# Optimization experiments

Measured on AMD Instinct MI355X. Metric: run time of the kernel, lower is better.

Reference implementation:

```python
import jax, jax.numpy as jnp
import numpy as np
from jax import lax

STATE_SIZE = 80
HIDDEN = 512
NC = 1
H = W = 32
STEPS = 64  # steps_range=(64,64)
THRESH = 0.01


def _maxpool3(x):
    # MaxPool2d(3, stride=1, padding=1) on NCHW
    return lax.reduce_window(x, -jnp.inf, lax.max, (1, 1, 3, 3), (1, 1, 1, 1), 'SAME')


def _conv3x3(x, w, b):
    y = lax.conv_general_dilated(x, w, (1, 1), 'SAME',
                                 dimension_numbers=('NCHW', 'OIHW', 'NCHW'))
    return y + b[None, :, None, None]


def _conv1x1(x, w, b):
    # w: (O, I, 1, 1) -> pointwise einsum
    return jnp.einsum('oi,bihw->bohw', w[:, :, 0, 0], x) + b[None, :, None, None]


def setup_inputs() -> dict:
    key = jax.random.key(0)
    ks = jax.random.split(key, 7)
    z = jax.random.normal(ks[0], (8, 100, 1, 1), dtype=jnp.float32)
    W1 = jax.random.normal(ks[1], (HIDDEN, STATE_SIZE, 3, 3), jnp.float32) / np.sqrt(STATE_SIZE * 9)
    b1 = jax.random.normal(ks[2], (HIDDEN,), jnp.float32) * 0.01
    W2 = jax.random.normal(ks[3], (HIDDEN, HIDDEN, 1, 1), jnp.float32) / np.sqrt(HIDDEN)
    b2 = jax.random.normal(ks[4], (HIDDEN,), jnp.float32) * 0.01
    # original code zero-inits the last conv; use small random weights so grads flow
    W3 = jax.random.normal(ks[5], (STATE_SIZE, HIDDEN, 1, 1), jnp.float32) * (0.01 / np.sqrt(HIDDEN))
    b3 = jax.random.normal(ks[6], (STATE_SIZE,), jnp.float32) * 0.001
    return {'z': z, 'W1': W1, 'b1': b1, 'W2': W2, 'b2': b2, 'W3': W3, 'b3': b3}


def _forward(z, W1, b1, W2, b2, W3, b3):
    N = z.shape[0]
    cH, cW = H // 2, W // 2
    state = jnp.zeros((N, STATE_SIZE, H, W), dtype=z.dtype)
    init_hidden = z[:, :STATE_SIZE - 1, 0, 0]  # (N, 79)
    state = state.at[:, 1:, cH, cW].set(init_hidden)
    state = state.at[:, 0, cH, cW].set(1.0)

    keys = jax.random.split(jax.random.key(42), STEPS)

    def ca_step(state, step_key):
        pre_living = _maxpool3(state[:, 0:1]) > THRESH
        perception = _conv3x3(state, W1, b1)
        h = jax.nn.relu(_conv1x1(perception, W2, b2))
        updates = _conv1x1(h, W3, b3)
        # stochastic update with p=1 (rand < 1 is always True, kept for fidelity)
        mask = jax.random.uniform(step_key, (state.shape[0], 1, H, W)) < 1.0
        state = state + mask.astype(state.dtype) * updates
        post_living = _maxpool3(state[:, 0:1]) > THRESH
        living = (post_living & pre_living).astype(state.dtype)
        return state * living, None

    state, _ = lax.scan(ca_step, state, keys)
    return state[:, :NC]  # (N, 1, H, W)


def reference(z, W1, b1, W2, b2, W3, b3):
    return _forward(z, W1, b1, W2, b2, W3, b3)
```

## Files before the change

kernel.cpp:

```cpp
#include <hip/hip_runtime.h>


#define NPIX 8192
#define T_ALIVE 0.01f

typedef _Float16 f16;
typedef __attribute__((ext_vector_type(8)))  _Float16 h8_t;
typedef __attribute__((ext_vector_type(4)))  _Float16 h4_t;
typedef __attribute__((ext_vector_type(16))) float    fx16;

__global__ __launch_bounds__(256) void tr512(
    const float* __restrict__ W2, float* __restrict__ W2T)
{
    __shared__ float t[32][33];
    const int bx = blockIdx.x & 15, by = blockIdx.x >> 4;
    const int x = threadIdx.x & 31, y8 = threadIdx.x >> 5;
#pragma unroll
    for (int r = 0; r < 32; r += 8)
        t[r + y8][x] = W2[(size_t)(by * 32 + r + y8) * 512 + bx * 32 + x];
    __syncthreads();
#pragma unroll
    for (int r = 0; r < 32; r += 8)
        W2T[(size_t)(bx * 32 + r + y8) * 512 + by * 32 + x] = t[x][r + y8];
}

__global__ __launch_bounds__(256) void wc32(
    const float* __restrict__ W2T, const float* __restrict__ W1,
    float* __restrict__ Wc)
{
    __shared__ float As[16][32];
    __shared__ float Bs[16][32];
    const int tid = threadIdx.x;
    const int ty = tid >> 3, tx = tid & 7;
    const int m0 = blockIdx.y * 32, n0 = blockIdx.x * 32;
    float acc[4] = {0.f, 0.f, 0.f, 0.f};

    for (int k0 = 0; k0 < 512; k0 += 16) {
#pragma unroll
        for (int t = 0; t < 2; ++t) {
            const int idx = tid + t * 256;
            const int r = idx >> 5, c = idx & 31;
            As[r][c] = W2T[(size_t)(k0 + r) * 512 + m0 + c];
            const int n = n0 + c;
            Bs[r][c] = (n < 720) ? W1[(size_t)(k0 + r) * 720 + n] : 0.f;
        }
        __syncthreads();
#pragma unroll
        for (int kk = 0; kk < 16; ++kk) {
            const float a = As[kk][ty];
#pragma unroll
            for (int j = 0; j < 4; ++j)
                acc[j] = fmaf(a, Bs[kk][tx * 4 + j], acc[j]);
        }
        __syncthreads();
    }
    const int m = m0 + ty;
#pragma unroll
    for (int j = 0; j < 4; ++j) {
        const int n = n0 + tx * 4 + j;
        if (n < 720) Wc[(size_t)m * 720 + n] = acc[j];
    }
}

__global__ __launch_bounds__(256) void bc_k(
    const float* __restrict__ W2, const float* __restrict__ b1,
    const float* __restrict__ b2, float* __restrict__ bc)
{
    const int m = blockIdx.x * 256 + threadIdx.x;
    if (m >= 512) return;
    float a = b2[m];
    for (int h = 0; h < 512; ++h) a += W2[m * 512 + h] * b1[h];
    bc[m] = a;
}

__global__ __launch_bounds__(256) void swz_wc2(
    const float* __restrict__ Wc, f16* __restrict__ Wcsw2)
{
    const int idx = blockIdx.x * 256 + threadIdx.x;
    if (idx >= 45 * 16 * 64) return;
    const int lane = idx & 63;
    const int t = idx >> 6;
    const int mtg = t & 15, ks = t >> 4;
    const int m = mtg * 32 + (lane & 31);
    const int k0 = ks * 16 + (lane >> 5) * 8;
    h8_t v;
#pragma unroll
    for (int j = 0; j < 8; ++j) {
        const int kp = k0 + j;
        const int tap = kp / 80, ci = kp - tap * 80;
        v[j] = (f16)Wc[(size_t)m * 720 + ci * 9 + tap];
    }
    *(h8_t*)(Wcsw2 + (size_t)idx * 8) = v;
}

__global__ __launch_bounds__(256) void swz_w32(
    const float* __restrict__ W3, f16* __restrict__ W3sw2)
{
    const int idx = blockIdx.x * 256 + threadIdx.x;
    if (idx >= 32 * 3 * 64) return;
    const int lane = idx & 63;
    const int t = idx >> 6;
    const int mt = t % 3, ks2 = t / 3;
    const int m = mt * 32 + (lane & 31);
    const int k0 = ks2 * 16 + (lane >> 5) * 8;
    h8_t v;
#pragma unroll
    for (int j = 0; j < 8; ++j)
        v[j] = (f16)((m < 80) ? W3[(size_t)m * 512 + k0 + j] : 0.f);
    *(h8_t*)(W3sw2 + (size_t)idx * 8) = v;
}

__global__ __launch_bounds__(256) void seed2(
    const float* __restrict__ z, float* __restrict__ U0,
    float* __restrict__ A0)
{
    const int idx = blockIdx.x * 256 + threadIdx.x;
    if (idx >= 640) return;
    const int b = idx / 80, c = idx - b * 80;
    const int n = b * 1024 + 16 * 32 + 16;
    const float v = (c == 0) ? 1.f : z[b * 100 + (c - 1)];
    U0[(size_t)c * NPIX + n] = v;
    if (c == 0) A0[n] = 1.f;
}

__global__ __launch_bounds__(1024) void kS(
    const f16* __restrict__ Wcsw2, const float* __restrict__ bc,
    const f16* __restrict__ W3sw2, const float* __restrict__ b3,
    const float* __restrict__ Uin, const float* __restrict__ Ain,
    float* __restrict__ Uout, float* __restrict__ Aout)
{
    __shared__ f16   msT[10880];
    __shared__ f16   Hsw[32768];
    __shared__ float bcL[512];
    __shared__ float b3L[80];
    __shared__ float SrowL[2][2560];
    __shared__ float N6[192];
    __shared__ float A6[192];
    __shared__ float live4[128];

    const int tid = threadIdx.x;
    const int lane = tid & 63, w = tid >> 6;
    const int li = lane & 31, q2 = lane >> 5;
    const int blk = blockIdx.x;
    const int b = blk >> 4, yg = blk & 15;
    const int y0 = yg * 2;
    const int gb = b * 1024;

    h8_t aring[6];
#pragma unroll
    for (int pk = 0; pk < 6; ++pk)
        aring[pk] = *(const h8_t*)(Wcsw2 +
            (((size_t)pk * 16 + w) * 64 + lane) * 8);

    if (tid < 512) bcL[tid] = bc[tid];
    if (tid < 80)  b3L[tid] = b3[tid];

    if (tid < 192) {
        const int r = tid >> 5, x = tid & 31, yy = y0 - 2 + r;
        const bool ok = ((unsigned)yy < 32u);
        N6[tid] = ok ? Uin[gb + yy * 32 + x] : -1e30f;
        A6[tid] = ok ? Ain[gb + yy * 32 + x] : -1e30f;
    }
    if (tid < 80) {
        const int cc = tid >> 3, rem = tid & 7;
        const int r = rem >> 1, xi = (rem & 1) * 33;
        h8_t zz;
#pragma unroll
        for (int j = 0; j < 8; ++j) zz[j] = (f16)0.f;
        *(h8_t*)(msT + (size_t)(cc * 136 + r * 34 + xi) * 8) = zz;
    }
    __syncthreads();

    if (tid < 128) {
        const int r = tid >> 5, x = tid & 31;
        float mN = -1e30f, mA = -1e30f;
#pragma unroll
        for (int rr = 0; rr < 3; ++rr)
#pragma unroll
            for (int dx = -1; dx <= 1; ++dx) {
                const int xx = x + dx;
                if ((unsigned)xx < 32u) {
                    mN = fmaxf(mN, N6[(r + rr) * 32 + xx]);
                    mA = fmaxf(mA, A6[(r + rr) * 32 + xx]);
                }
            }
        live4[tid] = (mN > T_ALIVE && mA > T_ALIVE) ? 1.f : 0.f;
    }
    __syncthreads();

#pragma unroll
    for (int it = 0; it < 10; ++it) {
        const int e = tid + it * 1024;
        const int x = e & 31;
        const int t2 = e >> 5;
        const int r = t2 / 80, ch = t2 - r * 80;
        const int yy = y0 - 1 + r;
        float v = 0.f;
        if ((unsigned)yy < 32u)
            v = Uin[(size_t)ch * NPIX + gb + yy * 32 + x] * live4[r * 32 + x];
        msT[(size_t)((ch >> 3) * 136 + r * 34 + x + 1) * 8 + (ch & 7)] = (f16)v;
        if (r == 1 || r == 2) {
            SrowL[r - 1][ch * 32 + x] = v;
            if (ch == 0) Aout[gb + (y0 + r - 1) * 32 + x] = v;
        }
    }
    __syncthreads();

    int pxh[9];
#pragma unroll
    for (int t = 0; t < 9; ++t)
        pxh[t] = ((t / 3) * 34 + li + (t % 3)) * 8;

    fx16 acc0, acc1;
#pragma unroll
    for (int r = 0; r < 16; ++r) { acc0[r] = 0.f; acc1[r] = 0.f; }

#pragma unroll
    for (int ks = 0; ks < 45; ++ks) {
        const int o0 = 2 * ks, o1 = 2 * ks + 1;
        const int a0 = (o0 % 10) * 1088 + pxh[o0 / 10];
        const int a1 = (o1 % 10) * 1088 + pxh[o1 / 10];
        const int ab = q2 ? a1 : a0;
        const h8_t bf0 = *(const h8_t*)(msT + ab);
        const h8_t bf1 = *(const h8_t*)(msT + ab + 272);
        const h8_t av = aring[ks % 6];
        if (ks + 6 < 45)
            aring[ks % 6] = *(const h8_t*)(Wcsw2 +
                (((size_t)(ks + 6) * 16 + w) * 64 + lane) * 8);
        acc0 = __builtin_amdgcn_mfma_f32_32x32x16_f16(av, bf0, acc0, 0, 0, 0);
        acc1 = __builtin_amdgcn_mfma_f32_32x32x16_f16(av, bf1, acc1, 0, 0, 0);
    }

#pragma unroll
    for (int aa = 0; aa < 4; ++aa) {
        const int chl = 8 * aa + 4 * q2;
        const int co = w * 4 + aa;
        h4_t v0, v1;
#pragma unroll
        for (int rb = 0; rb < 4; ++rb) {
            const float bb = bcL[w * 32 + chl + rb];
            v0[rb] = (f16)fmaxf(acc0[aa * 4 + rb] + bb, 0.f);
            v1[rb] = (f16)fmaxf(acc1[aa * 4 + rb] + bb, 0.f);
        }
        *(h4_t*)(Hsw + ((size_t)co * 64 +      li) * 8 + 4 * q2) = v0;
        *(h4_t*)(Hsw + ((size_t)co * 64 + 32 + li) * 8 + 4 * q2) = v1;
    }
    __syncthreads();

    if (w < 6) {
        const int mt = w >> 1, r = w & 1;
        h8_t ar[8];
#pragma unroll
        for (int pk = 0; pk < 8; ++pk)
            ar[pk] = *(const h8_t*)(W3sw2 +
                (((size_t)pk * 3 + mt) * 64 + lane) * 8);

        fx16 acc3;
#pragma unroll
        for (int rr = 0; rr < 16; ++rr) acc3[rr] = 0.f;
#pragma unroll
        for (int ks2 = 0; ks2 < 32; ++ks2) {
            const h8_t bf = *(const h8_t*)(Hsw +
                ((size_t)(ks2 * 2 + q2) * 64 + r * 32 + li) * 8);
            const h8_t a = ar[ks2 & 7];
            if (ks2 + 8 < 32)
                ar[ks2 & 7] = *(const h8_t*)(W3sw2 +
                    (((size_t)(ks2 + 8) * 3 + mt) * 64 + lane) * 8);
            acc3 = __builtin_amdgcn_mfma_f32_32x32x16_f16(a, bf, acc3, 0, 0, 0);
        }

        const size_t px = (size_t)(gb + (y0 + r) * 32 + li);
#pragma unroll
        for (int aa = 0; aa < 4; ++aa)
#pragma unroll
            for (int rb = 0; rb < 4; ++rb) {
                const int ch = mt * 32 + rb + 8 * aa + 4 * q2;
                if (ch < 80) {
                    Uout[(size_t)ch * NPIX + px] =
                        SrowL[r][ch * 32 + li] + acc3[aa * 4 + rb] + b3L[ch];
                }
            }
    }
}

__global__ __launch_bounds__(128) void kF(
    const float* __restrict__ Uf, const float* __restrict__ Af,
    float* __restrict__ dout)
{
    __shared__ float N3[96];
    __shared__ float A3[96];
    const int tid = threadIdx.x;
    const int blk = blockIdx.x;
    const int b = blk >> 5, y = blk & 31;
    const int gb = b * 1024;

    if (tid < 96) {
        const int r = tid >> 5, x = tid & 31, yy = y - 1 + r;
        const bool ok = ((unsigned)yy < 32u);
        N3[tid] = ok ? Uf[gb + yy * 32 + x] : -1e30f;
        A3[tid] = ok ? Af[gb + yy * 32 + x] : -1e30f;
    }
    __syncthreads();

    if (tid < 32) {
        float mN = -1e30f, mA = -1e30f;
#pragma unroll
        for (int rr = 0; rr < 3; ++rr)
#pragma unroll
            for (int dx = -1; dx <= 1; ++dx) {
                const int xx = tid + dx;
                if ((unsigned)xx < 32u) {
                    mN = fmaxf(mN, N3[rr * 32 + xx]);
                    mA = fmaxf(mA, A3[rr * 32 + xx]);
                }
            }
        const float lv = (mN > T_ALIVE && mA > T_ALIVE) ? 1.f : 0.f;
        dout[gb + y * 32 + tid] = Uf[gb + y * 32 + tid] * lv;
    }
}

extern "C" void kernel_launch(void* const* d_in, const int* in_sizes, int n_in,
                              void* d_out, int out_size, void* d_ws, size_t ws_size,
                              hipStream_t stream)
{
    const float* z  = (const float*)d_in[0];
    const float* W1 = (const float*)d_in[1];
    const float* b1 = (const float*)d_in[2];
    const float* W2 = (const float*)d_in[3];
    const float* b2 = (const float*)d_in[4];
    const float* W3 = (const float*)d_in[5];
    const float* b3 = (const float*)d_in[6];

    char* ws = (char*)d_ws;
    float* U0    = (float*)ws;  ws += (size_t)80 * NPIX * 4;
    float* U1    = (float*)ws;  ws += (size_t)80 * NPIX * 4;
    float* A0    = (float*)ws;  ws += (size_t)NPIX * 4;
    float* A1    = (float*)ws;  ws += (size_t)NPIX * 4;
    float* bc    = (float*)ws;  ws += 512 * 4;
    float* Wc    = (float*)ws;  ws += (size_t)512 * 720 * 4;
    float* W2T   = (float*)ws;  ws += (size_t)512 * 512 * 4;
    f16*   Wcsw2 = (f16*)ws;   ws += (size_t)45 * 16 * 64 * 8 * 2;
    f16*   W3sw2 = (f16*)ws;   ws += (size_t)32 * 3 * 64 * 8 * 2;

    hipMemsetAsync(U0, 0, (size_t)80 * NPIX * 4, stream);
    hipMemsetAsync(A0, 0, (size_t)NPIX * 4, stream);
    seed2<<<3, 256, 0, stream>>>(z, U0, A0);
    tr512<<<256, 256, 0, stream>>>(W2, W2T);
    wc32<<<dim3(23, 16), 256, 0, stream>>>(W2T, W1, Wc);
    bc_k<<<2, 256, 0, stream>>>(W2, b1, b2, bc);
    swz_wc2<<<180, 256, 0, stream>>>(Wc, Wcsw2);
    swz_w32<<<24, 256, 0, stream>>>(W3, W3sw2);

    float* Uc = U0;  float* Un = U1;
    float* Ac = A0;  float* An = A1;
    for (int s = 0; s < 64; ++s) {
        kS<<<128, 1024, 0, stream>>>(Wcsw2, bc, W3sw2, b3, Uc, Ac, Un, An);
        float* t = Uc; Uc = Un; Un = t;
        float* a = Ac; Ac = An; An = a;
    }
    kF<<<256, 128, 0, stream>>>(Uc, Ac, (float*)d_out);
}
```

Measured before the change: 1.294 ms.

## Split hidden dimension across two blocks with partial-sum state buffers

Each step kernel now launches 256 blocks of 512 threads instead of 128 blocks of 1024, with each block pair splitting the 512 hidden channels in half. Each half computes its share of the fused conv and its partial W3 projection. Half 0 writes the state plus bias and half 1 writes its partial update into a second buffer, and the next step sums the two on load. This is meant to use more CUs on the 256-CU device, at the cost of duplicated input staging, an extra full-size state buffer read and written each step, and slightly more register pressure from a deeper weight prefetch ring.

```diff
diff --git a/kernel.cpp b/kernel.cpp
--- a/kernel.cpp
+++ b/kernel.cpp
@@ -123,15 +123,17 @@
     if (c == 0) A0[n] = 1.f;
 }
 
-__global__ __launch_bounds__(1024) void kS(
+__global__ __launch_bounds__(512) void kS(
     const f16* __restrict__ Wcsw2, const float* __restrict__ bc,
     const f16* __restrict__ W3sw2, const float* __restrict__ b3,
-    const float* __restrict__ Uin, const float* __restrict__ Ain,
-    float* __restrict__ Uout, float* __restrict__ Aout)
+    const float* __restrict__ Uin, const float* __restrict__ Upin,
+    const float* __restrict__ Ain,
+    float* __restrict__ Uout, float* __restrict__ Upout,
+    float* __restrict__ Aout)
 {
     __shared__ f16   msT[10880];
-    __shared__ f16   Hsw[32768];
-    __shared__ float bcL[512];
+    __shared__ f16   Hsw[16384];
+    __shared__ float bcL[256];
     __shared__ float b3L[80];
     __shared__ float SrowL[2][2560];
     __shared__ float N6[192];
@@ -142,24 +144,26 @@
     const int lane = tid & 63, w = tid >> 6;
     const int li = lane & 31, q2 = lane >> 5;
     const int blk = blockIdx.x;
-    const int b = blk >> 4, yg = blk & 15;
-    const int y0 = yg * 2;
+    const int half = blk & 1, g = blk >> 1;
+    const int b = g >> 4, y0 = (g & 15) * 2;
     const int gb = b * 1024;
-
-    h8_t aring[6];
-#pragma unroll
-    for (int pk = 0; pk < 6; ++pk)
+    const int mt = half * 8 + w;
+
+    h8_t aring[8];
+#pragma unroll
+    for (int pk = 0; pk < 8; ++pk)
         aring[pk] = *(const h8_t*)(Wcsw2 +
-            (((size_t)pk * 16 + w) * 64 + lane) * 8);
-
-    if (tid < 512) bcL[tid] = bc[tid];
+            (((size_t)pk * 16 + mt) * 64 + lane) * 8);
+
+    if (tid < 256) bcL[tid] = bc[half * 256 + tid];
     if (tid < 80)  b3L[tid] = b3[tid];
 
     if (tid < 192) {
         const int r = tid >> 5, x = tid & 31, yy = y0 - 2 + r;
         const bool ok = ((unsigned)yy < 32u);
-        N6[tid] = ok ? Uin[gb + yy * 32 + x] : -1e30f;
-        A6[tid] = ok ? Ain[gb + yy * 32 + x] : -1e30f;
+        const int o = gb + yy * 32 + x;
+        N6[tid] = ok ? (Uin[o] + Upin[o]) : -1e30f;
+        A6[tid] = ok ? Ain[o] : -1e30f;
     }
     if (tid < 80) {
         const int cc = tid >> 3, rem = tid & 7;
@@ -189,19 +193,21 @@
     __syncthreads();
 
 #pragma unroll
-    for (int it = 0; it < 10; ++it) {
-        const int e = tid + it * 1024;
+    for (int it = 0; it < 20; ++it) {
+        const int e = tid + it * 512;
         const int x = e & 31;
         const int t2 = e >> 5;
         const int r = t2 / 80, ch = t2 - r * 80;
         const int yy = y0 - 1 + r;
         float v = 0.f;
-        if ((unsigned)yy < 32u)
-            v = Uin[(size_t)ch * NPIX + gb + yy * 32 + x] * live4[r * 32 + x];
+        if ((unsigned)yy < 32u) {
+            const size_t o = (size_t)ch * NPIX + gb + yy * 32 + x;
+            v = (Uin[o] + Upin[o]) * live4[r * 32 + x];
+        }
         msT[(size_t)((ch >> 3) * 136 + r * 34 + x + 1) * 8 + (ch & 7)] = (f16)v;
         if (r == 1 || r == 2) {
             SrowL[r - 1][ch * 32 + x] = v;
-            if (ch == 0) Aout[gb + (y0 + r - 1) * 32 + x] = v;
+            if (ch == 0 && half == 0) Aout[gb + (y0 + r - 1) * 32 + x] = v;
         }
     }
     __syncthreads();
@@ -217,16 +223,14 @@
 
 #pragma unroll
     for (int ks = 0; ks < 45; ++ks) {
-        const int o0 = 2 * ks, o1 = 2 * ks + 1;
-        const int a0 = (o0 % 10) * 1088 + pxh[o0 / 10];
-        const int a1 = (o1 % 10) * 1088 + pxh[o1 / 10];
-        const int ab = q2 ? a1 : a0;
+        const int o = 2 * ks + q2;
+        const int ab = (o % 10) * 1088 + pxh[o / 10];
         const h8_t bf0 = *(const h8_t*)(msT + ab);
         const h8_t bf1 = *(const h8_t*)(msT + ab + 272);
-        const h8_t av = aring[ks % 6];
-        if (ks + 6 < 45)
-            aring[ks % 6] = *(const h8_t*)(Wcsw2 +
-                (((size_t)(ks + 6) * 16 + w) * 64 + lane) * 8);
+        const h8_t av = aring[ks & 7];
+        if (ks + 8 < 45)
+            aring[ks & 7] = *(const h8_t*)(Wcsw2 +
+                (((size_t)(ks + 8) * 16 + mt) * 64 + lane) * 8);
         acc0 = __builtin_amdgcn_mfma_f32_32x32x16_f16(av, bf0, acc0, 0, 0, 0);
         acc1 = __builtin_amdgcn_mfma_f32_32x32x16_f16(av, bf1, acc1, 0, 0, 0);
     }
@@ -248,24 +252,24 @@
     __syncthreads();
 
     if (w < 6) {
-        const int mt = w >> 1, r = w & 1;
+        const int m3 = w >> 1, r = w & 1;
         h8_t ar[8];
 #pragma unroll
         for (int pk = 0; pk < 8; ++pk)
             ar[pk] = *(const h8_t*)(W3sw2 +
-                (((size_t)pk * 3 + mt) * 64 + lane) * 8);
+                (((size_t)(half * 16 + pk) * 3 + m3) * 64 + lane) * 8);
 
         fx16 acc3;
 #pragma unroll
         for (int rr = 0; rr < 16; ++rr) acc3[rr] = 0.f;
 #pragma unroll
-        for (int ks2 = 0; ks2 < 32; ++ks2) {
+        for (int i = 0; i < 16; ++i) {
             const h8_t bf = *(const h8_t*)(Hsw +
-                ((size_t)(ks2 * 2 + q2) * 64 + r * 32 + li) * 8);
-            const h8_t a = ar[ks2 & 7];
-            if (ks2 + 8 < 32)
-                ar[ks2 & 7] = *(const h8_t*)(W3sw2 +
-                    (((size_t)(ks2 + 8) * 3 + mt) * 64 + lane) * 8);
+                ((size_t)(i * 2 + q2) * 64 + r * 32 + li) * 8);
+            const h8_t a = ar[i & 7];
+            if (i + 8 < 16)
+                ar[i & 7] = *(const h8_t*)(W3sw2 +
+                    (((size_t)(half * 16 + i + 8) * 3 + m3) * 64 + lane) * 8);
             acc3 = __builtin_amdgcn_mfma_f32_32x32x16_f16(a, bf, acc3, 0, 0, 0);
         }
 
@@ -274,18 +278,22 @@
         for (int aa = 0; aa < 4; ++aa)
 #pragma unroll
             for (int rb = 0; rb < 4; ++rb) {
-                const int ch = mt * 32 + rb + 8 * aa + 4 * q2;
+                const int ch = m3 * 32 + rb + 8 * aa + 4 * q2;
                 if (ch < 80) {
-                    Uout[(size_t)ch * NPIX + px] =
-                        SrowL[r][ch * 32 + li] + acc3[aa * 4 + rb] + b3L[ch];
+                    const size_t idx = (size_t)ch * NPIX + px;
+                    if (half == 0)
+                        Uout[idx] = SrowL[r][ch * 32 + li]
+                                  + acc3[aa * 4 + rb] + b3L[ch];
+                    else
+                        Upout[idx] = acc3[aa * 4 + rb];
                 }
             }
     }
 }
 
 __global__ __launch_bounds__(128) void kF(
-    const float* __restrict__ Uf, const float* __restrict__ Af,
-    float* __restrict__ dout)
+    const float* __restrict__ Uf, const float* __restrict__ Upf,
+    const float* __restrict__ Af, float* __restrict__ dout)
 {
     __shared__ float N3[96];
     __shared__ float A3[96];
@@ -297,8 +305,9 @@
     if (tid < 96) {
         const int r = tid >> 5, x = tid & 31, yy = y - 1 + r;
         const bool ok = ((unsigned)yy < 32u);
-        N3[tid] = ok ? Uf[gb + yy * 32 + x] : -1e30f;
-        A3[tid] = ok ? Af[gb + yy * 32 + x] : -1e30f;
+        const int o = gb + yy * 32 + x;
+        N3[tid] = ok ? (Uf[o] + Upf[o]) : -1e30f;
+        A3[tid] = ok ? Af[o] : -1e30f;
     }
     __syncthreads();
 
@@ -315,7 +324,8 @@
                 }
             }
         const float lv = (mN > T_ALIVE && mA > T_ALIVE) ? 1.f : 0.f;
-        dout[gb + y * 32 + tid] = Uf[gb + y * 32 + tid] * lv;
+        const int o = gb + y * 32 + tid;
+        dout[o] = (Uf[o] + Upf[o]) * lv;
     }
 }
 
@@ -334,6 +344,8 @@
     char* ws = (char*)d_ws;
     float* U0    = (float*)ws;  ws += (size_t)80 * NPIX * 4;
     float* U1    = (float*)ws;  ws += (size_t)80 * NPIX * 4;
+    float* Up0   = (float*)ws;  ws += (size_t)80 * NPIX * 4;
+    float* Up1   = (float*)ws;  ws += (size_t)80 * NPIX * 4;
     float* A0    = (float*)ws;  ws += (size_t)NPIX * 4;
     float* A1    = (float*)ws;  ws += (size_t)NPIX * 4;
     float* bc    = (float*)ws;  ws += 512 * 4;
@@ -343,6 +355,7 @@
     f16*   W3sw2 = (f16*)ws;   ws += (size_t)32 * 3 * 64 * 8 * 2;
 
     hipMemsetAsync(U0, 0, (size_t)80 * NPIX * 4, stream);
+    hipMemsetAsync(Up0, 0, (size_t)80 * NPIX * 4, stream);
     hipMemsetAsync(A0, 0, (size_t)NPIX * 4, stream);
     seed2<<<3, 256, 0, stream>>>(z, U0, A0);
     tr512<<<256, 256, 0, stream>>>(W2, W2T);
@@ -351,12 +364,16 @@
     swz_wc2<<<180, 256, 0, stream>>>(Wc, Wcsw2);
     swz_w32<<<24, 256, 0, stream>>>(W3, W3sw2);
 
-    float* Uc = U0;  float* Un = U1;
-    float* Ac = A0;  float* An = A1;
+    float* Uc = U0;   float* Un = U1;
+    float* Upc = Up0; float* Upn = Up1;
+    float* Ac = A0;   float* An = A1;
     for (int s = 0; s < 64; ++s) {
-        kS<<<128, 1024, 0, stream>>>(Wcsw2, bc, W3sw2, b3, Uc, Ac, Un, An);
-        float* t = Uc; Uc = Un; Un = t;
-        float* a = Ac; Ac = An; An = a;
-    }
-    kF<<<256, 128, 0, stream>>>(Uc, Ac, (float*)d_out);
-}
+        kS<<<256, 512, 0, stream>>>(Wcsw2, bc, W3sw2, b3,
+                                    Uc, Upc, Ac, Un, Upn, An);
+        float* t;
+        t = Uc;  Uc = Un;   Un = t;
+        t = Upc; Upc = Upn; Upn = t;
+        t = Ac;  Ac = An;   An = t;
+    }
+    kF<<<256, 128, 0, stream>>>(Uc, Upc, Ac, (float*)d_out);
+}
```

Result: faster. 1.156 ms (-10.7%).
